# Performance work log

Hardware: AMD Instinct MI355X
Metric: run time of the kernel (lower is better)

The kernel has to match this reference:

```python
import jax, jax.numpy as jnp
import numpy as np

B, S, HID = 2, 2048, 4096
H, KV, D = 32, 8, 128  # query heads, kv heads, head_dim
ROPE_BASE = 10000.0


def apply_rope(x, cos, sin):
    # x: (B, h, S, D); cos/sin: (S, D) broadcast over (B, h)
    x1 = x[..., ::2]
    x2 = x[..., 1::2]
    rotated = jnp.stack((-x2, x1), axis=-1).reshape(x.shape)  # interleave back
    return x * cos + rotated * sin


def setup_inputs() -> dict:
    key = jax.random.key(0)
    ks = jax.random.split(key, 5)
    hidden_states = jax.random.normal(ks[0], (B, S, HID), jnp.float32)
    # real rotary tables (interleaved convention: each freq repeated twice)
    inv_freq = 1.0 / (ROPE_BASE ** (jnp.arange(0, D, 2, dtype=jnp.float32) / D))
    freqs = jnp.arange(S, dtype=jnp.float32)[:, None] * inv_freq  # (S, D/2)
    freqs = jnp.repeat(freqs, 2, axis=-1)  # (S, D)
    cos, sin = jnp.cos(freqs), jnp.sin(freqs)
    std = 0.02
    wq = jax.random.normal(ks[1], (H * D, HID), jnp.float32) * std
    wk = jax.random.normal(ks[2], (KV * D, HID), jnp.float32) * std
    wv = jax.random.normal(ks[3], (KV * D, HID), jnp.float32) * std
    wo = jax.random.normal(ks[4], (HID, H * D), jnp.float32) * std
    return {"hidden_states": hidden_states, "cos": cos, "sin": sin,
            "wq": wq, "wk": wk, "wv": wv, "wo": wo}


def reference(hidden_states, cos, sin, wq, wk, wv, wo):
    bsz, seq, _ = hidden_states.shape
    G = H // KV  # GQA group size
    q = (hidden_states @ wq.T).reshape(bsz, seq, H, D).transpose(0, 2, 1, 3)   # (B,H,S,D)
    k = (hidden_states @ wk.T).reshape(bsz, seq, KV, D).transpose(0, 2, 1, 3)  # (B,KV,S,D)
    v = (hidden_states @ wv.T).reshape(bsz, seq, KV, D).transpose(0, 2, 1, 3)
    q = apply_rope(q, cos, sin)
    k = apply_rope(k, cos, sin)
    # GQA without materializing repeated K/V: group query heads per KV head
    qg = q.reshape(bsz, KV, G, seq, D)
    scale = 1.0 / np.float32(np.sqrt(D))
    scores = jnp.einsum('bkgsd,bktd->bkgst', qg, k) * scale  # (B,KV,G,S,S)
    causal = jnp.tril(jnp.ones((seq, seq), bool))
    scores = jnp.where(causal, scores, jnp.finfo(scores.dtype).min)
    probs = jax.nn.softmax(scores, axis=-1)
    attn = jnp.einsum('bkgst,bktd->bkgsd', probs, v)  # (B,KV,G,S,D)
    attn = attn.reshape(bsz, H, seq, D).transpose(0, 2, 1, 3).reshape(bsz, seq, H * D)
    return attn @ wo.T
```

## Files before the change

kernel.cpp:

```cpp
#include <hip/hip_runtime.h>

typedef unsigned short u16;
typedef unsigned int u32;
using bf8 = __attribute__((ext_vector_type(8))) short;
using f4  = __attribute__((ext_vector_type(4))) float;

#define DEV __device__ __forceinline__

#define QSCALE (0.08838834764831845f * 1.4426950408889634f)

DEV u16 f2b(float f) {
  u32 u = __float_as_uint(f);
  u32 r = u + 0x7fff + ((u >> 16) & 1);
  return (u16)(r >> 16);
}
DEV u32 f2b_u(u32 u) {
  return (u + 0x7fff + ((u >> 16) & 1)) >> 16;
}
DEV float b2f(u32 bits) { return __uint_as_float(bits << 16); }

#define GLOAD16(g, l)                                                          \
  __builtin_amdgcn_global_load_lds((__attribute__((address_space(1))) u32*)(g),\
                                   (__attribute__((address_space(3))) u32*)(l),\
                                   16, 0, 0)

DEV f4 mfma16(bf8 a, bf8 b, f4 c) {
  return __builtin_amdgcn_mfma_f32_16x16x32_bf16(a, b, c, 0, 0, 0);
}

__global__ __launch_bounds__(256) void convert_kernel(
    const u16* __restrict__ src, u16* __restrict__ dst,
    const u32* __restrict__ probe, int n8) {
  const int t = blockIdx.x * 256 + threadIdx.x;
  if (t >= n8) return;
  const bool isf32 = (probe[0] == 0x3F800000u);
  const uint4* s4 = (const uint4*)src;
  uint4* d4 = (uint4*)dst;
  if (!isf32) {
    d4[t] = s4[t];
    return;
  }
  uint4 a = s4[2 * t];
  uint4 b = s4[2 * t + 1];
  uint4 o;
  o.x = f2b_u(a.x) | (f2b_u(a.y) << 16);
  o.y = f2b_u(a.z) | (f2b_u(a.w) << 16);
  o.z = f2b_u(b.x) | (f2b_u(b.y) << 16);
  o.w = f2b_u(b.z) | (f2b_u(b.w) << 16);
  d4[t] = o;
}

DEV void gemm_core(const u16* __restrict__ A, const u16* __restrict__ W,
                   int lda, int ldw, int K, int mb, int nb,
                   u16* As, u16* Bs, f4 (&acc)[4][4]) {
  const int tid = threadIdx.x;
  const int lane = tid & 63;
  const int wid = tid >> 6;
  const int l16 = lane & 15;
  const int quad = lane >> 4;
  const int wm = (wid >> 1) * 64;
  const int wn = (wid & 1) * 64;

  const int c0 = wid * 2;
  const int rowA0 = c0 * 16 + (lane >> 2);
  const int colb = (lane & 3) * 16;

  const char* gA = (const char*)(A + (size_t)(mb * 128 + rowA0) * lda) + colb;
  const char* gB = (const char*)(W + (size_t)(nb * 128 + rowA0) * ldw) + colb;
  char* lA = (char*)As + c0 * 1024;
  char* lB = (char*)Bs + c0 * 1024;
  const size_t strideA = (size_t)lda * 32;
  const size_t strideB = (size_t)ldw * 32;

  for (int k0 = 0; k0 < K; k0 += 32) {
    __syncthreads();
    GLOAD16(gA + (size_t)k0 * 2, lA);
    GLOAD16(gA + (size_t)k0 * 2 + strideA, lA + 1024);
    GLOAD16(gB + (size_t)k0 * 2, lB);
    GLOAD16(gB + (size_t)k0 * 2 + strideB, lB + 1024);
    __syncthreads();

    bf8 af[4], bw[4];
#pragma unroll
    for (int t = 0; t < 4; t++) {
      af[t] = *(const bf8*)(As + (wm + t * 16 + l16) * 32 + quad * 8);
      bw[t] = *(const bf8*)(Bs + (wn + t * 16 + l16) * 32 + quad * 8);
    }
#pragma unroll
    for (int mt = 0; mt < 4; mt++)
#pragma unroll
      for (int nt = 0; nt < 4; nt++)
        acc[mt][nt] = mfma16(af[mt], bw[nt], acc[mt][nt]);
  }
}

__global__ __launch_bounds__(256) void gemm_qkv_kernel(
    const u16* __restrict__ hidden, const u16* __restrict__ wq,
    const u16* __restrict__ wk, const u16* __restrict__ wv,
    u16* __restrict__ qo, u16* __restrict__ ko, u16* __restrict__ vto) {
  __shared__ u16 As[128 * 32];
  __shared__ u16 Bs[128 * 32];
  const int mb = blockIdx.x, yb = blockIdx.y;
  const u16* W;
  u16* C;
  int nb, ldc, mode;
  if (yb < 32)      { W = wq; C = qo;  nb = yb;      ldc = 4096; mode = 0; }
  else if (yb < 40) { W = wk; C = ko;  nb = yb - 32; ldc = 1024; mode = 0; }
  else              { W = wv; C = vto; nb = yb - 40; ldc = 0;    mode = 1; }

  f4 acc[4][4];
#pragma unroll
  for (int i = 0; i < 4; i++)
#pragma unroll
    for (int j = 0; j < 4; j++) acc[i][j] = (f4){0.f, 0.f, 0.f, 0.f};

  gemm_core(hidden, W, 4096, 4096, 4096, mb, nb, As, Bs, acc);

  const int tid = threadIdx.x, lane = tid & 63, wid = tid >> 6;
  const int l16 = lane & 15, quad = lane >> 4;
  const int wm = (wid >> 1) * 64, wn = (wid & 1) * 64;

  if (mode == 0) {
#pragma unroll
    for (int mt = 0; mt < 4; mt++)
#pragma unroll
      for (int nt = 0; nt < 4; nt++) {
        const int n = nb * 128 + wn + nt * 16 + l16;
        const int m0 = mb * 128 + wm + mt * 16 + quad * 4;
#pragma unroll
        for (int r = 0; r < 4; r++)
          C[(size_t)(m0 + r) * ldc + n] = f2b(acc[mt][nt][r]);
      }
  } else {
#pragma unroll
    for (int mt = 0; mt < 4; mt++)
#pragma unroll
      for (int nt = 0; nt < 4; nt++) {
        const int n = nb * 128 + wn + nt * 16 + l16;
        const int m0 = mb * 128 + wm + mt * 16 + quad * 4;
        const int b_ = m0 >> 11, s0 = m0 & 2047;
        ushort4 pk;
        pk.x = f2b(acc[mt][nt][0]);
        pk.y = f2b(acc[mt][nt][1]);
        pk.z = f2b(acc[mt][nt][2]);
        pk.w = f2b(acc[mt][nt][3]);
        *(ushort4*)(vto + ((size_t)(b_ * 1024 + n) << 11) + s0) = pk;
      }
  }
}

__global__ __launch_bounds__(256) void gemm_o_kernel(
    const u16* __restrict__ A, const u16* __restrict__ W,
    float* __restrict__ C) {
  __shared__ u16 As[128 * 32];
  __shared__ u16 Bs[128 * 32];
  const int mb = blockIdx.x, nb = blockIdx.y;
  f4 acc[4][4];
#pragma unroll
  for (int i = 0; i < 4; i++)
#pragma unroll
    for (int j = 0; j < 4; j++) acc[i][j] = (f4){0.f, 0.f, 0.f, 0.f};

  gemm_core(A, W, 4096, 4096, 4096, mb, nb, As, Bs, acc);

  const int tid = threadIdx.x, lane = tid & 63, wid = tid >> 6;
  const int l16 = lane & 15, quad = lane >> 4;
  const int wm = (wid >> 1) * 64, wn = (wid & 1) * 64;
#pragma unroll
  for (int mt = 0; mt < 4; mt++)
#pragma unroll
    for (int nt = 0; nt < 4; nt++) {
      const int n = nb * 128 + wn + nt * 16 + l16;
      const int m0 = mb * 128 + wm + mt * 16 + quad * 4;
#pragma unroll
      for (int r = 0; r < 4; r++)
        C[(size_t)(m0 + r) * 4096 + n] = acc[mt][nt][r];
    }
}

__global__ void rope_kernel(u16* __restrict__ x, const u16* __restrict__ cs,
                            const u16* __restrict__ sn, int shift, float scale,
                            int nthreads) {
  const int t = blockIdx.x * 256 + threadIdx.x;
  if (t >= nthreads) return;
  const size_t e = (size_t)t * 8;
  const int d = (int)(e & 127);
  const int s = (int)((e >> shift) & 2047);
  uint4 xv = *(const uint4*)(x + e);
  uint4 cv = *(const uint4*)(cs + (size_t)s * 128 + d);
  uint4 sv = *(const uint4*)(sn + (size_t)s * 128 + d);
  u32 xw[4] = {xv.x, xv.y, xv.z, xv.w};
  u32 cw[4] = {cv.x, cv.y, cv.z, cv.w};
  u32 sw[4] = {sv.x, sv.y, sv.z, sv.w};
  u32 ow[4];
#pragma unroll
  for (int i = 0; i < 4; i++) {
    float x0 = b2f(xw[i] & 0xffff), x1 = b2f(xw[i] >> 16);
    float c = b2f(cw[i] & 0xffff);
    float si = b2f(sw[i] & 0xffff);
    float o0 = (x0 * c - x1 * si) * scale;
    float o1 = (x1 * c + x0 * si) * scale;
    ow[i] = (u32)f2b(o0) | ((u32)f2b(o1) << 16);
  }
  uint4 ov = {ow[0], ow[1], ow[2], ow[3]};
  *(uint4*)(x + e) = ov;
}

__global__ __launch_bounds__(256) void attn_kernel(
    const u16* __restrict__ q, const u16* __restrict__ k,
    const u16* __restrict__ vt, u16* __restrict__ attn) {
  __shared__ u16 Ks[64 * 136];
  __shared__ u16 Vt[128 * 72];
  __shared__ u16 Ps[4][16 * 72];

  const int qblk = blockIdx.x, h = blockIdx.y, b = blockIdx.z;
  const int kv = h >> 2;
  const int tid = threadIdx.x, lane = tid & 63, wid = tid >> 6;
  const int l16 = lane & 15, quad = lane >> 4;

  const u16* qp =
      q + ((size_t)(b * 2048 + qblk * 64 + wid * 16 + l16) * 32 + h) * 128;
  bf8 aq[4];
#pragma unroll
  for (int ds = 0; ds < 4; ds++)
    aq[ds] = *(const bf8*)(qp + ds * 32 + quad * 8);

  f4 accO[8];
#pragma unroll
  for (int i = 0; i < 8; i++) accO[i] = (f4){0.f, 0.f, 0.f, 0.f};
  float mrow[4] = {-1e30f, -1e30f, -1e30f, -1e30f};
  float lrow[4] = {0.f, 0.f, 0.f, 0.f};

  const u16* kp = k + ((size_t)(b * 2048) * 8 + kv) * 128;
  const u16* vp = vt + (size_t)(b * 8 + kv) * 128 * 2048;

  const int qg = qblk * 64 + wid * 16 + quad * 4;

  for (int kt = 0; kt <= qblk; kt++) {
    const int key0 = kt * 64;
    __syncthreads();
#pragma unroll
    for (int rep = 0; rep < 4; rep++) {
      const int e = rep * 2048 + tid * 8;
      const int row = e >> 7, col = e & 127;
      *(uint4*)(Ks + row * 136 + col) =
          *(const uint4*)(kp + (size_t)(key0 + row) * 1024 + col);
    }
#pragma unroll
    for (int rep = 0; rep < 4; rep++) {
      const int e = rep * 2048 + tid * 8;
      const int row = e >> 6, col = e & 63;
      *(uint4*)(Vt + row * 72 + col) =
          *(const uint4*)(vp + (size_t)row * 2048 + key0 + col);
    }
    __syncthreads();

    f4 sc[4];
#pragma unroll
    for (int nt = 0; nt < 4; nt++) {
      sc[nt] = (f4){0.f, 0.f, 0.f, 0.f};
      const int krow = nt * 16 + l16;
#pragma unroll
      for (int ds = 0; ds < 4; ds++) {
        bf8 bk = *(const bf8*)(Ks + krow * 136 + ds * 32 + quad * 8);
        sc[nt] = mfma16(aq[ds], bk, sc[nt]);
      }
    }

    u16 pbits[4][4];
#pragma unroll
    for (int r = 0; r < 4; r++) {
      float mx = -1e30f;
#pragma unroll
      for (int nt = 0; nt < 4; nt++) {
        const int keyg = key0 + nt * 16 + l16;
        if (keyg > qg + r) sc[nt][r] = -1e30f;
        mx = fmaxf(mx, sc[nt][r]);
      }
#pragma unroll
      for (int off = 1; off < 16; off <<= 1)
        mx = fmaxf(mx, __shfl_xor(mx, off, 64));
      const float mn = fmaxf(mrow[r], mx);
      const float alpha = exp2f(mrow[r] - mn);
      mrow[r] = mn;
      float ps = 0.f;
#pragma unroll
      for (int nt = 0; nt < 4; nt++) {
        const float p = exp2f(sc[nt][r] - mn);
        ps += p;
        pbits[nt][r] = f2b(p);
      }
#pragma unroll
      for (int off = 1; off < 16; off <<= 1) ps += __shfl_xor(ps, off, 64);
      lrow[r] = lrow[r] * alpha + ps;
#pragma unroll
      for (int nt = 0; nt < 8; nt++) accO[nt][r] *= alpha;
    }

#pragma unroll
    for (int nt = 0; nt < 4; nt++)
#pragma unroll
      for (int r = 0; r < 4; r++)
        Ps[wid][(quad * 4 + r) * 72 + nt * 16 + l16] = pbits[nt][r];
    __syncthreads();

#pragma unroll
    for (int ks = 0; ks < 2; ks++) {
      bf8 ap = *(const bf8*)(&Ps[wid][l16 * 72 + ks * 32 + quad * 8]);
#pragma unroll
      for (int nt = 0; nt < 8; nt++) {
        bf8 bv = *(const bf8*)(Vt + (nt * 16 + l16) * 72 + ks * 32 + quad * 8);
        accO[nt] = mfma16(ap, bv, accO[nt]);
      }
    }
  }

  float inv[4];
#pragma unroll
  for (int r = 0; r < 4; r++) inv[r] = 1.0f / lrow[r];
#pragma unroll
  for (int nt = 0; nt < 8; nt++)
#pragma unroll
    for (int r = 0; r < 4; r++) {
      const int s = qblk * 64 + wid * 16 + quad * 4 + r;
      const int dcol = nt * 16 + l16;
      attn[((size_t)(b * 2048 + s) * 32 + h) * 128 + dcol] =
          f2b(accO[nt][r] * inv[r]);
    }
}

extern "C" void kernel_launch(void* const* d_in, const int* in_sizes, int n_in,
                              void* d_out, int out_size, void* d_ws,
                              size_t ws_size, hipStream_t stream) {
  const u16* hidden = (const u16*)d_in[0];
  const u16* cosp = (const u16*)d_in[1];
  const u16* sinp = (const u16*)d_in[2];
  const u16* wq = (const u16*)d_in[3];
  const u16* wk = (const u16*)d_in[4];
  const u16* wv = (const u16*)d_in[5];
  const u16* wo = (const u16*)d_in[6];
  const u32* probe = (const u32*)d_in[1];
  float* out = (float*)d_out;

  char* ws = (char*)d_ws;
  u16* hidden_n = (u16*)(ws);
  u16* attnb    = (u16*)(ws);
  u16* qb       = (u16*)(ws + 33554432);
  u16* kb       = (u16*)(ws + 67108864);
  u16* vtb      = (u16*)(ws + 75497472);
  u16* wq_n     = (u16*)(ws + 83886080);
  u16* wk_n     = (u16*)(ws + 117440512);
  u16* wv_n     = (u16*)(ws + 125829120);
  u16* wo_n     = (u16*)(ws + 134217728);
  u16* cos_n    = (u16*)(ws + 167772160);
  u16* sin_n    = (u16*)(ws + 168296448);

  dim3 blk(256);
  convert_kernel<<<dim3(8192), blk, 0, stream>>>(hidden, hidden_n, probe,
                                                 2097152);
  convert_kernel<<<dim3(8192), blk, 0, stream>>>(wq, wq_n, probe, 2097152);
  convert_kernel<<<dim3(2048), blk, 0, stream>>>(wk, wk_n, probe, 524288);
  convert_kernel<<<dim3(2048), blk, 0, stream>>>(wv, wv_n, probe, 524288);
  convert_kernel<<<dim3(8192), blk, 0, stream>>>(wo, wo_n, probe, 2097152);
  convert_kernel<<<dim3(128), blk, 0, stream>>>(cosp, cos_n, probe, 32768);
  convert_kernel<<<dim3(128), blk, 0, stream>>>(sinp, sin_n, probe, 32768);

  gemm_qkv_kernel<<<dim3(32, 48), blk, 0, stream>>>(hidden_n, wq_n, wk_n, wv_n,
                                                    qb, kb, vtb);
  rope_kernel<<<dim3(8192), blk, 0, stream>>>(qb, cos_n, sin_n, 12, QSCALE,
                                              2097152);
  rope_kernel<<<dim3(2048), blk, 0, stream>>>(kb, cos_n, sin_n, 10, 1.0f,
                                              524288);
  attn_kernel<<<dim3(32, 32, 2), blk, 0, stream>>>(qb, kb, vtb, attnb);
  gemm_o_kernel<<<dim3(32, 32), blk, 0, stream>>>(attnb, wo_n, out);
}
```

Baseline: 1.094 ms.

## Share K/V tiles across GQA head group per block in attention

The attention kernel now launches one block per KV head instead of per query head, with each of the four waves handling one query head of the GQA group over 64 query rows. Each K/V tile loaded into shared memory is therefore reused by four heads, cutting global K/V traffic fourfold. It also pairs short and long causal query blocks in the grid order to balance load, replaces shuffle reductions with DPP row rotations, applies the causal mask only on the diagonal tile, and drops a block-wide barrier. In exchange each thread holds far more registers (4x8 accumulators plus Q fragments), which limits occupancy and may spill, and the grid has a quarter as many blocks.

```diff
diff --git a/kernel.cpp b/kernel.cpp
--- a/kernel.cpp
+++ b/kernel.cpp
@@ -26,6 +26,24 @@
 
 DEV f4 mfma16(bf8 a, bf8 b, f4 c) {
   return __builtin_amdgcn_mfma_f32_16x16x32_bf16(a, b, c, 0, 0, 0);
+}
+
+#define ROR_F(x, n)                                                            \
+  __int_as_float(__builtin_amdgcn_update_dpp(                                  \
+      0, __float_as_int(x), 0x120 + (n), 0xf, 0xf, true))
+DEV float rowmax16(float x) {
+  x = fmaxf(x, ROR_F(x, 1));
+  x = fmaxf(x, ROR_F(x, 2));
+  x = fmaxf(x, ROR_F(x, 4));
+  x = fmaxf(x, ROR_F(x, 8));
+  return x;
+}
+DEV float rowsum16(float x) {
+  x += ROR_F(x, 1);
+  x += ROR_F(x, 2);
+  x += ROR_F(x, 4);
+  x += ROR_F(x, 8);
+  return x;
 }
 
 __global__ __launch_bounds__(256) void convert_kernel(
@@ -206,35 +224,47 @@
   *(uint4*)(x + e) = ov;
 }
 
-__global__ __launch_bounds__(256) void attn_kernel(
+__global__ __launch_bounds__(256, 2) void attn_kernel(
     const u16* __restrict__ q, const u16* __restrict__ k,
     const u16* __restrict__ vt, u16* __restrict__ attn) {
   __shared__ u16 Ks[64 * 136];
   __shared__ u16 Vt[128 * 72];
-  __shared__ u16 Ps[4][16 * 72];
-
-  const int qblk = blockIdx.x, h = blockIdx.y, b = blockIdx.z;
-  const int kv = h >> 2;
+  __shared__ u16 Ps[4][64 * 72];
+
+  const int bx = blockIdx.x;
+  const int qblk = (bx & 1) ? (31 - (bx >> 1)) : (bx >> 1);
+  const int kv = blockIdx.y, b = blockIdx.z;
   const int tid = threadIdx.x, lane = tid & 63, wid = tid >> 6;
   const int l16 = lane & 15, quad = lane >> 4;
-
-  const u16* qp =
-      q + ((size_t)(b * 2048 + qblk * 64 + wid * 16 + l16) * 32 + h) * 128;
-  bf8 aq[4];
-#pragma unroll
-  for (int ds = 0; ds < 4; ds++)
-    aq[ds] = *(const bf8*)(qp + ds * 32 + quad * 8);
-
-  f4 accO[8];
-#pragma unroll
-  for (int i = 0; i < 8; i++) accO[i] = (f4){0.f, 0.f, 0.f, 0.f};
-  float mrow[4] = {-1e30f, -1e30f, -1e30f, -1e30f};
-  float lrow[4] = {0.f, 0.f, 0.f, 0.f};
+  const int h = kv * 4 + wid;
+
+  bf8 aq[4][4];
+  const u16* qbase = q + ((size_t)(b * 2048 + qblk * 64) * 32 + h) * 128;
+#pragma unroll
+  for (int mt = 0; mt < 4; mt++) {
+    const u16* qp = qbase + (size_t)(mt * 16 + l16) * 4096;
+#pragma unroll
+    for (int ks = 0; ks < 4; ks++)
+      aq[mt][ks] = *(const bf8*)(qp + ks * 32 + quad * 8);
+  }
+
+  f4 accO[4][8];
+#pragma unroll
+  for (int i = 0; i < 4; i++)
+#pragma unroll
+    for (int j = 0; j < 8; j++) accO[i][j] = (f4){0.f, 0.f, 0.f, 0.f};
+  float mrow[4][4], lrow[4][4];
+#pragma unroll
+  for (int i = 0; i < 4; i++)
+#pragma unroll
+    for (int r = 0; r < 4; r++) {
+      mrow[i][r] = -1e30f;
+      lrow[i][r] = 0.f;
+    }
 
   const u16* kp = k + ((size_t)(b * 2048) * 8 + kv) * 128;
   const u16* vp = vt + (size_t)(b * 8 + kv) * 128 * 2048;
-
-  const int qg = qblk * 64 + wid * 16 + quad * 4;
+  u16* Pw = Ps[wid];
 
   for (int kt = 0; kt <= qblk; kt++) {
     const int key0 = kt * 64;
@@ -255,78 +285,81 @@
     }
     __syncthreads();
 
-    f4 sc[4];
-#pragma unroll
-    for (int nt = 0; nt < 4; nt++) {
-      sc[nt] = (f4){0.f, 0.f, 0.f, 0.f};
-      const int krow = nt * 16 + l16;
-#pragma unroll
-      for (int ds = 0; ds < 4; ds++) {
-        bf8 bk = *(const bf8*)(Ks + krow * 136 + ds * 32 + quad * 8);
-        sc[nt] = mfma16(aq[ds], bk, sc[nt]);
+    const bool diag = (kt == qblk);
+
+#pragma unroll
+    for (int mt = 0; mt < 4; mt++) {
+      f4 sc[4];
+#pragma unroll
+      for (int nt = 0; nt < 4; nt++) sc[nt] = (f4){0.f, 0.f, 0.f, 0.f};
+#pragma unroll
+      for (int ks = 0; ks < 4; ks++)
+#pragma unroll
+        for (int nt = 0; nt < 4; nt++) {
+          bf8 bk = *(const bf8*)(Ks + (nt * 16 + l16) * 136 + ks * 32 +
+                                 quad * 8);
+          sc[nt] = mfma16(aq[mt][ks], bk, sc[nt]);
+        }
+
+      const int qrow = mt * 16 + quad * 4;
+#pragma unroll
+      for (int r = 0; r < 4; r++) {
+        if (diag) {
+#pragma unroll
+          for (int nt = 0; nt < 4; nt++)
+            if (nt * 16 + l16 > qrow + r) sc[nt][r] = -1e30f;
+        }
+        float mx = fmaxf(fmaxf(sc[0][r], sc[1][r]), fmaxf(sc[2][r], sc[3][r]));
+        mx = rowmax16(mx);
+        const float mn = fmaxf(mrow[mt][r], mx);
+        const float alpha = exp2f(mrow[mt][r] - mn);
+        mrow[mt][r] = mn;
+        float p0 = exp2f(sc[0][r] - mn);
+        float p1 = exp2f(sc[1][r] - mn);
+        float p2 = exp2f(sc[2][r] - mn);
+        float p3 = exp2f(sc[3][r] - mn);
+        float ps = rowsum16((p0 + p1) + (p2 + p3));
+        lrow[mt][r] = lrow[mt][r] * alpha + ps;
+#pragma unroll
+        for (int nd = 0; nd < 8; nd++) accO[mt][nd][r] *= alpha;
+        Pw[(qrow + r) * 72 + 0 * 16 + l16] = f2b(p0);
+        Pw[(qrow + r) * 72 + 1 * 16 + l16] = f2b(p1);
+        Pw[(qrow + r) * 72 + 2 * 16 + l16] = f2b(p2);
+        Pw[(qrow + r) * 72 + 3 * 16 + l16] = f2b(p3);
       }
     }
 
-    u16 pbits[4][4];
-#pragma unroll
-    for (int r = 0; r < 4; r++) {
-      float mx = -1e30f;
-#pragma unroll
-      for (int nt = 0; nt < 4; nt++) {
-        const int keyg = key0 + nt * 16 + l16;
-        if (keyg > qg + r) sc[nt][r] = -1e30f;
-        mx = fmaxf(mx, sc[nt][r]);
+#pragma unroll
+    for (int ks2 = 0; ks2 < 2; ks2++) {
+      bf8 ap[4];
+#pragma unroll
+      for (int mt = 0; mt < 4; mt++)
+        ap[mt] = *(const bf8*)(Pw + (mt * 16 + l16) * 72 + ks2 * 32 + quad * 8);
+#pragma unroll
+      for (int nd = 0; nd < 8; nd++) {
+        bf8 bv = *(const bf8*)(Vt + (nd * 16 + l16) * 72 + ks2 * 32 + quad * 8);
+#pragma unroll
+        for (int mt = 0; mt < 4; mt++)
+          accO[mt][nd] = mfma16(ap[mt], bv, accO[mt][nd]);
       }
-#pragma unroll
-      for (int off = 1; off < 16; off <<= 1)
-        mx = fmaxf(mx, __shfl_xor(mx, off, 64));
-      const float mn = fmaxf(mrow[r], mx);
-      const float alpha = exp2f(mrow[r] - mn);
-      mrow[r] = mn;
-      float ps = 0.f;
-#pragma unroll
-      for (int nt = 0; nt < 4; nt++) {
-        const float p = exp2f(sc[nt][r] - mn);
-        ps += p;
-        pbits[nt][r] = f2b(p);
+    }
+  }
+
+#pragma unroll
+  for (int mt = 0; mt < 4; mt++) {
+    float inv[4];
+#pragma unroll
+    for (int r = 0; r < 4; r++) inv[r] = 1.0f / lrow[mt][r];
+#pragma unroll
+    for (int nd = 0; nd < 8; nd++)
+#pragma unroll
+      for (int r = 0; r < 4; r++) {
+        const int s = qblk * 64 + mt * 16 + quad * 4 + r;
+        const int dcol = nd * 16 + l16;
+        attn[((size_t)(b * 2048 + s) * 32 + h) * 128 + dcol] =
+            f2b(accO[mt][nd][r] * inv[r]);
       }
-#pragma unroll
-      for (int off = 1; off < 16; off <<= 1) ps += __shfl_xor(ps, off, 64);
-      lrow[r] = lrow[r] * alpha + ps;
-#pragma unroll
-      for (int nt = 0; nt < 8; nt++) accO[nt][r] *= alpha;
-    }
-
-#pragma unroll
-    for (int nt = 0; nt < 4; nt++)
-#pragma unroll
-      for (int r = 0; r < 4; r++)
-        Ps[wid][(quad * 4 + r) * 72 + nt * 16 + l16] = pbits[nt][r];
-    __syncthreads();
-
-#pragma unroll
-    for (int ks = 0; ks < 2; ks++) {
-      bf8 ap = *(const bf8*)(&Ps[wid][l16 * 72 + ks * 32 + quad * 8]);
-#pragma unroll
-      for (int nt = 0; nt < 8; nt++) {
-        bf8 bv = *(const bf8*)(Vt + (nt * 16 + l16) * 72 + ks * 32 + quad * 8);
-        accO[nt] = mfma16(ap, bv, accO[nt]);
-      }
-    }
-  }
-
-  float inv[4];
-#pragma unroll
-  for (int r = 0; r < 4; r++) inv[r] = 1.0f / lrow[r];
-#pragma unroll
-  for (int nt = 0; nt < 8; nt++)
-#pragma unroll
-    for (int r = 0; r < 4; r++) {
-      const int s = qblk * 64 + wid * 16 + quad * 4 + r;
-      const int dcol = nt * 16 + l16;
-      attn[((size_t)(b * 2048 + s) * 32 + h) * 128 + dcol] =
-          f2b(accO[nt][r] * inv[r]);
-    }
+  }
 }
 
 extern "C" void kernel_launch(void* const* d_in, const int* in_sizes, int n_in,
@@ -371,6 +404,6 @@
                                               2097152);
   rope_kernel<<<dim3(2048), blk, 0, stream>>>(kb, cos_n, sin_n, 10, 1.0f,
                                               524288);
-  attn_kernel<<<dim3(32, 32, 2), blk, 0, stream>>>(qb, kb, vtb, attnb);
+  attn_kernel<<<dim3(32, 8, 2), blk, 0, stream>>>(qb, kb, vtb, attnb);
   gemm_o_kernel<<<dim3(32, 32), blk, 0, stream>>>(attnb, wo_n, out);
 }
```

Measured after the change: 1.363 ms. +24.6%, slower.
